# Kernel tuning notes

Hardware: AMD Instinct MI355X
Metric: run time of the kernel (lower is better)

Reference implementation:

```python
import jax, jax.numpy as jnp
import numpy as np

N_HEADS = 16

def setup_inputs() -> dict:
    key = jax.random.key(0)
    ks = jax.random.split(key, 9)
    B, L, D = 4, 2048, 1024
    s = D ** -0.5
    return {
        "x": jax.random.normal(ks[0], (B, L, D), dtype=jnp.float32),
        "Wq": jax.random.normal(ks[1], (D, D), dtype=jnp.float32) * s,
        "bq": jax.random.normal(ks[2], (D,), dtype=jnp.float32) * 0.02,
        "Wk": jax.random.normal(ks[3], (D, D), dtype=jnp.float32) * s,
        "bk": jax.random.normal(ks[4], (D,), dtype=jnp.float32) * 0.02,
        "Wv": jax.random.normal(ks[5], (D, D), dtype=jnp.float32) * s,
        "bv": jax.random.normal(ks[6], (D,), dtype=jnp.float32) * 0.02,
        "Wo": jax.random.normal(ks[7], (D, D), dtype=jnp.float32) * s,
        "bo": jax.random.normal(ks[8], (D,), dtype=jnp.float32) * 0.02,
    }

def reference(x, Wq, bq, Wk, bk, Wv, bv, Wo, bo):
    B, L, D = x.shape
    H = N_HEADS
    hd = D // H
    scale = hd ** -0.5
    # torch Linear: y = x @ W.T + b
    q = (x @ Wq.T + bq).reshape(B, L, H, hd)
    k = (x @ Wk.T + bk).reshape(B, L, H, hd)
    v = (x @ Wv.T + bv).reshape(B, L, H, hd)
    # scores [B,H,L,L]
    qk = jnp.einsum('bqhd,bkhd->bhqk', q, k) * scale
    causal = jnp.tril(jnp.ones((L, L), dtype=bool))
    qk = jnp.where(causal[None, None, :, :], qk, -jnp.inf)
    attn = jax.nn.softmax(qk, axis=-1)
    out = jnp.einsum('bhqk,bkhd->bqhd', attn, v).reshape(B, L, D)
    return out @ Wo.T + bo
```

## Files before the change

kernel.cpp:

```cpp
#include <hip/hip_runtime.h>
#include <hip/hip_bf16.h>
#include <math.h>

#define Bsz 4
#define Lsz 2048
#define Dsz 1024
#define Hn 16
#define HDsz 64
#define NQT 16

typedef __attribute__((ext_vector_type(8))) short short8;
typedef __attribute__((ext_vector_type(4))) float floatx4;
typedef unsigned short ushort_t;

__device__ __forceinline__ void load_lds_16B(const void* g, void* l) {
    __builtin_amdgcn_global_load_lds(
        (const __attribute__((address_space(1))) unsigned int*)g,
        (__attribute__((address_space(3))) unsigned int*)l, 16, 0, 0);
}

__device__ inline void cvt_store(float* p, size_t i, float v) { p[i] = v; }
__device__ inline void cvt_store(__hip_bfloat16* p, size_t i, float v) {
    p[i] = __float2bfloat16(v);
}

__device__ inline ushort_t f2bf_raw(float f) {
    __hip_bfloat16 b = __float2bfloat16(f);
    return *reinterpret_cast<ushort_t*>(&b);
}

__device__ inline float bf2f_raw(ushort_t u) {
    union { unsigned int i; float f; } c;
    c.i = ((unsigned int)u) << 16;
    return c.f;
}

__device__ __forceinline__ float fast_exp2(float x) {
#if __has_builtin(__builtin_amdgcn_exp2f)
    return __builtin_amdgcn_exp2f(x);
#else
    return exp2f(x);
#endif
}

__device__ __forceinline__ unsigned pk_bf16_rhu(float p0, float p1) {
    return __builtin_amdgcn_perm(__builtin_bit_cast(unsigned, p1) + 0x8000u,
                                 __builtin_bit_cast(unsigned, p0) + 0x8000u,
                                 0x07060302u);
}

__global__ __launch_bounds__(256) void f2ball(
    const float* __restrict__ x, const float* __restrict__ w0,
    const float* __restrict__ w1, const float* __restrict__ w2,
    const float* __restrict__ w3, __hip_bfloat16* __restrict__ xb,
    __hip_bfloat16* __restrict__ wb) {
    int bid = blockIdx.x;
    const float* in;
    __hip_bfloat16* o;
    size_t off;
    if (bid < 8192) {
        off = (size_t)bid * 1024 + threadIdx.x * 4;
        in = x;
        o = xb + off;
    } else {
        int b2 = bid - 8192;
        int sel = b2 >> 10;
        in = sel == 0 ? w0 : (sel == 1 ? w1 : (sel == 2 ? w2 : w3));
        off = (size_t)(b2 & 1023) * 1024 + threadIdx.x * 4;
        o = wb + (size_t)sel * (1024 * 1024) + off;
    }
    float4 v = *(const float4*)(in + off);
    o[0] = __float2bfloat16(v.x);
    o[1] = __float2bfloat16(v.y);
    o[2] = __float2bfloat16(v.z);
    o[3] = __float2bfloat16(v.w);
}

template <typename TO, bool QKV>
__global__ __launch_bounds__(512, 2) void gemm_bt_256(
    const ushort_t* __restrict__ A, const ushort_t* __restrict__ W,
    const float* __restrict__ b0, const float* __restrict__ b1,
    const float* __restrict__ b2, TO* __restrict__ C, int M, int N, int K) {
    __shared__ ushort_t As[2][256 * 64];
    __shared__ ushort_t Bs[2][128 * 64];

    const int t = threadIdx.x;
    const int wave = t >> 6, lane = t & 63;
    const int lmod = lane & 15, quad = lane >> 4;
    const int wm = wave >> 2, wn = wave & 3;

    const int nbn = N >> 7;
    const int nwg = nbn * (M >> 8);
    const int bid = blockIdx.x;
    const int wg = (bid & 7) * (nwg >> 3) + (bid >> 3);
    const int n0 = (wg % nbn) * 128, m0 = (wg / nbn) * 256;

    floatx4 acc[2][2][4] = {};
    short8 Af[4][2], Bf[2];

    const int NT = K >> 6;

    auto stageA = [&](int kt, int bi) {
        const int kk = kt << 6;
#pragma unroll
        for (int p = 0; p < 4; p++) {
            int slot = t + p * 512;
            int row = slot >> 3, c8 = slot & 7;
            int gc8 = c8 ^ (row & 7);
            load_lds_16B(A + (size_t)(m0 + row) * K + kk + gc8 * 8,
                         &As[bi][slot * 8]);
        }
    };
    auto stageB = [&](int kt, int bi) {
        const int kk = kt << 6;
#pragma unroll
        for (int p = 0; p < 2; p++) {
            int slot = t + p * 512;
            int row = slot >> 3, c8 = slot & 7;
            int gc8 = c8 ^ (row & 7);
            load_lds_16B(W + (size_t)(n0 + row) * K + kk + gc8 * 8,
                         &Bs[bi][slot * 8]);
        }
    };
    auto rdA = [&](int bi, int mh) {
#pragma unroll
        for (int mr = 0; mr < 4; mr++) {
            int row = wm * 128 + mh * 64 + mr * 16 + lmod;
#pragma unroll
            for (int ks = 0; ks < 2; ks++) {
                int sc8 = (ks * 4 + quad) ^ (row & 7);
                Af[mr][ks] = *(const short8*)&As[bi][row * 64 + sc8 * 8];
            }
        }
    };
    auto rdB = [&](int bi, int nh) {
        int row = wn * 32 + nh * 16 + lmod;
#pragma unroll
        for (int ks = 0; ks < 2; ks++) {
            int sc8 = (ks * 4 + quad) ^ (row & 7);
            Bf[ks] = *(const short8*)&Bs[bi][row * 64 + sc8 * 8];
        }
    };
    auto domm = [&](int mh, int nh) {
        __builtin_amdgcn_s_setprio(1);
#pragma unroll
        for (int mr = 0; mr < 4; mr++)
#pragma unroll
            for (int ks = 0; ks < 2; ks++)
                acc[mh][nh][mr] = __builtin_amdgcn_mfma_f32_16x16x32_bf16(
                    Af[mr][ks], Bf[ks], acc[mh][nh][mr], 0, 0, 0);
        __builtin_amdgcn_s_setprio(0);
    };

    stageA(0, 0);
    stageB(0, 0);
    asm volatile("s_waitcnt vmcnt(0)" ::: "memory");
    __builtin_amdgcn_s_barrier();
    asm volatile("" ::: "memory");

#pragma unroll 1
    for (int T = 0; T < NT; T++) {
        const int cur = T & 1, nxt = cur ^ 1;
        const bool pf = (T + 1 < NT);
        rdA(cur, 0);
        rdB(cur, 0);
        if (pf) stageA(T + 1, nxt);
        __builtin_amdgcn_s_barrier();
        __builtin_amdgcn_sched_barrier(0);
        domm(0, 0);
        __builtin_amdgcn_s_barrier();
        rdB(cur, 1);
        if (pf) stageB(T + 1, nxt);
        __builtin_amdgcn_s_barrier();
        __builtin_amdgcn_sched_barrier(0);
        domm(0, 1);
        __builtin_amdgcn_s_barrier();
        rdA(cur, 1);
        __builtin_amdgcn_s_barrier();
        __builtin_amdgcn_sched_barrier(0);
        domm(1, 1);
        __builtin_amdgcn_s_barrier();
        rdB(cur, 0);
        __builtin_amdgcn_s_barrier();
        __builtin_amdgcn_sched_barrier(0);
        domm(1, 0);
        asm volatile("s_waitcnt vmcnt(0)" ::: "memory");
        __builtin_amdgcn_s_barrier();
        asm volatile("" ::: "memory");
    }

    const int sec = QKV ? (n0 >> 10) : 0;
    const float* bp = QKV ? (sec == 0 ? b0 : (sec == 1 ? b1 : b2)) : b0;
    TO* Cb = QKV ? (C + (size_t)sec * M * 1024) : C;
    const int Nout = QKV ? 1024 : N;
    const float sc = (QKV && sec == 0) ? 0.1803368801111204f : 1.0f;

#pragma unroll
    for (int mh = 0; mh < 2; mh++)
#pragma unroll
        for (int mr = 0; mr < 4; mr++) {
            int gm = m0 + wm * 128 + mh * 64 + mr * 16 + quad * 4;
#pragma unroll
            for (int nh = 0; nh < 2; nh++) {
                int gn = n0 + wn * 32 + nh * 16 + lmod;
                int cn = QKV ? (gn & 1023) : gn;
                float b = bp[cn];
#pragma unroll
                for (int r = 0; r < 4; r++)
                    cvt_store(Cb, (size_t)(gm + r) * Nout + cn,
                              (acc[mh][nh][mr][r] + b) * sc);
            }
        }
}

__global__ __launch_bounds__(256) void attn_mfma(
    const ushort_t* __restrict__ q, const ushort_t* __restrict__ k,
    const ushort_t* __restrict__ v, ushort_t* __restrict__ Opart,
    float* __restrict__ lpart) {
    __shared__ ushort_t Ks[2][64 * 64];
    __shared__ ushort_t Vts[64 * 64];
    __shared__ ushort_t Ps[4][32 * 64];

    const int t = threadIdx.x;
    const int wave = t >> 6, lane = t & 63;
    const int lmod = lane & 15, quad = lane >> 4;

    const int bid = blockIdx.x;
    const int j = bid >> 3;
    const int bx = j & 15;
    const int p = bx & 7, s = bx >> 3;
    const int bh = (bid & 7) + ((j >> 4) << 3);
    const int b = bh >> 4, h = bh & 15;
    const size_t base = ((size_t)b * Lsz) * Dsz + h * HDsz;

    const int vrp = t & 31, vcg = t >> 5;
    ushort_t* Pw = (ushort_t*)Ps[wave];
    const int lm7 = lmod & 7;

    auto stageK = [&](int kt, int bi) {
#pragma unroll
        for (int pp = 0; pp < 2; pp++) {
            int slot = t + pp * 256;
            int row = slot >> 3, c8 = slot & 7;
            int gc8 = c8 ^ (row & 7);
            load_lds_16B(k + base + (size_t)(kt * 64 + row) * Dsz + gc8 * 8,
                         &Ks[bi][slot * 8]);
        }
    };
    auto loadV = [&](int kt, uint4& r0, uint4& r1) {
        const ushort_t* v0p =
            v + base + (size_t)(kt * 64 + 2 * vrp) * Dsz + vcg * 8;
        r0 = *(const uint4*)v0p;
        r1 = *(const uint4*)(v0p + Dsz);
    };
    auto writeV = [&](uint4 r0, uint4 r1) {
        unsigned vv0[4] = {r0.x, r0.y, r0.z, r0.w};
        unsigned vv1[4] = {r1.x, r1.y, r1.z, r1.w};
        const int kk = 2 * vrp;
        const int kc8 = kk >> 3, klo = kk & 7;
#pragma unroll
        for (int jj = 0; jj < 4; jj++) {
            int d0 = vcg * 8 + 2 * jj;
            unsigned lo = __builtin_amdgcn_perm(vv1[jj], vv0[jj], 0x05040100u);
            unsigned hi = __builtin_amdgcn_perm(vv1[jj], vv0[jj], 0x07060302u);
            *(unsigned*)&Vts[d0 * 64 + (kc8 ^ (d0 & 7)) * 8 + klo] = lo;
            int d1 = d0 + 1;
            *(unsigned*)&Vts[d1 * 64 + (kc8 ^ (d1 & 7)) * 8 + klo] = hi;
        }
    };

    int bi = 0;
    uint4 vr0, vr1;

    {
        const int kt00 = s * (NQT - p);
        stageK(kt00, 0);
        loadV(kt00, vr0, vr1);
    }

#pragma unroll 1
    for (int seg = 0; seg < 2; seg++) {
        const int qtile = seg == 0 ? (NQT - 1 - p) : p;
        const int q0 = qtile * 128;
        const int Th = qtile + 1;
        const int kt0 = s * Th, kt1 = kt0 + Th;
        const int kt0n = s * (p + 1);

        short8 aq[2][2];
#pragma unroll
        for (int g = 0; g < 2; g++) {
            const ushort_t* qp = q + base +
                                 (size_t)(q0 + wave * 32 + g * 16 + lmod) * Dsz +
                                 quad * 8;
            aq[g][0] = *(const short8*)(qp);
            aq[g][1] = *(const short8*)(qp + 32);
        }

        floatx4 Oacc[2][4] = {};
        float lsum[2] = {0.f, 0.f};

#pragma unroll 1
        for (int kt = kt0; kt < kt1; kt++) {
            asm volatile("s_waitcnt vmcnt(0)" ::: "memory");
            __builtin_amdgcn_s_barrier();
            asm volatile("" ::: "memory");

            writeV(vr0, vr1);
            asm volatile("s_waitcnt lgkmcnt(0)" ::: "memory");
            __builtin_amdgcn_s_barrier();
            asm volatile("" ::: "memory");

            const int ktn = (kt + 1 < kt1) ? kt + 1 : (seg == 0 ? kt0n : -1);
            if (ktn >= 0) stageK(ktn, bi ^ 1);

            floatx4 St[2][4] = {};
#pragma unroll
            for (int nt = 0; nt < 4; nt++) {
                int key = nt * 16 + lmod;
#pragma unroll
                for (int ks = 0; ks < 2; ks++) {
                    int sc8 = (ks * 4 + quad) ^ (key & 7);
                    short8 kf = *(const short8*)&Ks[bi][(key * 8 + sc8) * 8];
#pragma unroll
                    for (int g = 0; g < 2; g++)
                        St[g][nt] = __builtin_amdgcn_mfma_f32_16x16x32_bf16(
                            kf, aq[g][ks], St[g][nt], 0, 0, 0);
                }
            }

            const bool need_mask = (kt >= 2 * qtile);
#pragma unroll
            for (int g = 0; g < 2; g++) {
                int qg = q0 + wave * 32 + g * 16 + lmod;
#pragma unroll
                for (int nt = 0; nt < 4; nt++) {
                    int k0g = kt * 64 + nt * 16 + quad * 4;
                    float p0 = fast_exp2(St[g][nt][0]);
                    float p1 = fast_exp2(St[g][nt][1]);
                    float p2 = fast_exp2(St[g][nt][2]);
                    float p3 = fast_exp2(St[g][nt][3]);
                    if (need_mask) {
                        if (k0g + 0 > qg) p0 = 0.f;
                        if (k0g + 1 > qg) p1 = 0.f;
                        if (k0g + 2 > qg) p2 = 0.f;
                        if (k0g + 3 > qg) p3 = 0.f;
                    }
                    lsum[g] += ((p0 + p1) + (p2 + p3));
                    uint2 w;
                    w.x = pk_bf16_rhu(p0, p1);
                    w.y = pk_bf16_rhu(p2, p3);
                    int c8 = nt * 2 + (quad >> 1);
                    int sc8 = c8 ^ lm7;
                    *(uint2*)&Pw[((g * 16 + lmod) * 8 + sc8) * 8 +
                                 (quad & 1) * 4] = w;
                }
            }

            if (ktn >= 0) loadV(ktn, vr0, vr1);

            short8 ap[2][2];
#pragma unroll
            for (int g = 0; g < 2; g++)
#pragma unroll
                for (int ks = 0; ks < 2; ks++) {
                    int sc8 = (ks * 4 + quad) ^ lm7;
                    ap[g][ks] =
                        *(const short8*)&Pw[((g * 16 + lmod) * 8 + sc8) * 8];
                }
#pragma unroll
            for (int on = 0; on < 4; on++) {
                int d = on * 16 + lmod;
#pragma unroll
                for (int ks = 0; ks < 2; ks++) {
                    int sc8 = (ks * 4 + quad) ^ (d & 7);
                    short8 bv = *(const short8*)&Vts[(d * 8 + sc8) * 8];
#pragma unroll
                    for (int g = 0; g < 2; g++)
                        Oacc[g][on] = __builtin_amdgcn_mfma_f32_16x16x32_bf16(
                            ap[g][ks], bv, Oacc[g][on], 0, 0, 0);
                }
            }

            bi ^= 1;
        }

#pragma unroll
        for (int g = 0; g < 2; g++) {
            lsum[g] += __shfl_xor(lsum[g], 16);
            lsum[g] += __shfl_xor(lsum[g], 32);
        }

        const size_t rec = ((size_t)bh * NQT + qtile) * 2 + s;
        ushort_t* Orec = Opart + rec * (128 * 64);
        float* lrec = lpart + rec * 128;
#pragma unroll
        for (int g = 0; g < 2; g++) {
            if (quad == 0) lrec[wave * 32 + g * 16 + lmod] = lsum[g];
#pragma unroll
            for (int r = 0; r < 4; r++) {
                int row = wave * 32 + g * 16 + quad * 4 + r;
#pragma unroll
                for (int on = 0; on < 4; on++) {
                    int d = on * 16 + lmod;
                    Orec[row * 64 + d] = f2bf_raw(Oacc[g][on][r]);
                }
            }
        }
    }
}

__global__ __launch_bounds__(256) void attn_combine(
    const ushort_t* __restrict__ Opart, const float* __restrict__ lpart,
    ushort_t* __restrict__ ao) {
    int gidx = blockIdx.x * 256 + threadIdx.x;
    int rowglob = gidx >> 3;
    int c8 = (gidx & 7) * 8;
    int bh = rowglob >> 11;
    int r11 = rowglob & 2047;
    int qtile = r11 >> 7, row = r11 & 127;

    size_t rec0 = ((size_t)bh * NQT + qtile) * 2;
    const ushort_t* O0 = Opart + (rec0 + 0) * (128 * 64) + row * 64 + c8;
    const ushort_t* O1 = Opart + (rec0 + 1) * (128 * 64) + row * 64 + c8;
    float l = lpart[(rec0 + 0) * 128 + row] + lpart[(rec0 + 1) * 128 + row];
    float inv = 1.0f / l;

    short8 a = *(const short8*)O0;
    short8 bvec = *(const short8*)O1;
    short8 o;
#pragma unroll
    for (int j = 0; j < 8; j++) {
        float vv = (bf2f_raw((ushort_t)a[j]) + bf2f_raw((ushort_t)bvec[j])) * inv;
        o[j] = (short)f2bf_raw(vv);
    }
    int b = bh >> 4, h = bh & 15;
    int qg = qtile * 128 + row;
    *(short8*)&ao[((size_t)(b * Lsz + qg)) * Dsz + h * HDsz + c8] = o;
}

extern "C" void kernel_launch(void* const* d_in, const int* in_sizes, int n_in,
                              void* d_out, int out_size, void* d_ws,
                              size_t ws_size, hipStream_t stream) {
    const size_t elems = (size_t)Bsz * Lsz * Dsz;
    const size_t welem = (size_t)Dsz * Dsz;
    const size_t nrec = (size_t)Bsz * Hn * NQT * 2;
    const size_t opart_e = nrec * 128 * 64;
    const size_t need = (5 * elems + 4 * welem + opart_e) * 2 + nrec * 128 * 4;
    if (ws_size < need) return;

    const float* x = (const float*)d_in[0];
    const float* Wq = (const float*)d_in[1];
    const float* bq = (const float*)d_in[2];
    const float* Wk = (const float*)d_in[3];
    const float* bk = (const float*)d_in[4];
    const float* Wv = (const float*)d_in[5];
    const float* bv = (const float*)d_in[6];
    const float* Wo = (const float*)d_in[7];
    const float* bo = (const float*)d_in[8];
    float* out = (float*)d_out;

    __hip_bfloat16* xb = (__hip_bfloat16*)d_ws;
    __hip_bfloat16* q = xb + elems;
    __hip_bfloat16* k = q + elems;
    __hip_bfloat16* v = k + elems;
    __hip_bfloat16* ao = v + elems;
    __hip_bfloat16* Wqb = ao + elems;
    __hip_bfloat16* Wkb = Wqb + welem;
    __hip_bfloat16* Wvb = Wkb + welem;
    __hip_bfloat16* Wob = Wvb + welem;
    ushort_t* Opart = (ushort_t*)(Wob + welem);
    float* lpart = (float*)(Opart + opart_e);

    const int M = Bsz * Lsz, N = Dsz, K = Dsz;

    f2ball<<<12288, 256, 0, stream>>>(x, Wq, Wk, Wv, Wo, xb, Wqb);

    gemm_bt_256<__hip_bfloat16, true><<<(3 * N / 128) * (M / 256), 512, 0,
                                        stream>>>(
        (const ushort_t*)xb, (const ushort_t*)Wqb, bq, bk, bv, q, M, 3 * N, K);

    attn_mfma<<<16 * Bsz * Hn, 256, 0, stream>>>(
        (const ushort_t*)q, (const ushort_t*)k, (const ushort_t*)v, Opart,
        lpart);

    attn_combine<<<(int)(elems / 8 / 256), 256, 0, stream>>>(Opart, lpart,
                                                             (ushort_t*)ao);

    gemm_bt_256<float, false><<<(N / 128) * (M / 256), 512, 0, stream>>>(
        (const ushort_t*)ao, (const ushort_t*)Wob, bo, bo, bo, out, M, N, K);
}
```

Before: 279.5 us.

## Stage V via async LDS loads and read transposed with ds_read_b64_tr_b16

V tiles were loaded into registers, transposed with perm instructions and written to LDS, which needed an extra barrier per key tile. They are now copied straight from global memory into a swizzled LDS buffer with global_load_lds, and the PV MFMA operands are read with the transposing ds_read_b64_tr_b16 instruction from precomputed addresses. Probability packing also switches from manual round-half-up to the hardware v_cvt_pk_bf16_f32 instruction. This removes VGPR staging and one barrier, but the V load is now issued in the same iteration it is consumed, with a vmcnt wait before PV, so less latency is hidden.

```diff
diff --git a/kernel.cpp b/kernel.cpp
--- a/kernel.cpp
+++ b/kernel.cpp
@@ -11,6 +11,7 @@
 
 typedef __attribute__((ext_vector_type(8))) short short8;
 typedef __attribute__((ext_vector_type(4))) float floatx4;
+typedef __attribute__((ext_vector_type(2))) unsigned uint2v;
 typedef unsigned short ushort_t;
 
 __device__ __forceinline__ void load_lds_16B(const void* g, void* l) {
@@ -41,12 +42,6 @@
 #else
     return exp2f(x);
 #endif
-}
-
-__device__ __forceinline__ unsigned pk_bf16_rhu(float p0, float p1) {
-    return __builtin_amdgcn_perm(__builtin_bit_cast(unsigned, p1) + 0x8000u,
-                                 __builtin_bit_cast(unsigned, p0) + 0x8000u,
-                                 0x07060302u);
 }
 
 __global__ __launch_bounds__(256) void f2ball(
@@ -218,7 +213,7 @@
     const ushort_t* __restrict__ v, ushort_t* __restrict__ Opart,
     float* __restrict__ lpart) {
     __shared__ ushort_t Ks[2][64 * 64];
-    __shared__ ushort_t Vts[64 * 64];
+    __shared__ ushort_t Vs[64 * 64];
     __shared__ ushort_t Ps[4][32 * 64];
 
     const int t = threadIdx.x;
@@ -233,7 +228,6 @@
     const int b = bh >> 4, h = bh & 15;
     const size_t base = ((size_t)b * Lsz) * Dsz + h * HDsz;
 
-    const int vrp = t & 31, vcg = t >> 5;
     ushort_t* Pw = (ushort_t*)Ps[wave];
     const int lm7 = lmod & 7;
 
@@ -247,36 +241,40 @@
                          &Ks[bi][slot * 8]);
         }
     };
-    auto loadV = [&](int kt, uint4& r0, uint4& r1) {
-        const ushort_t* v0p =
-            v + base + (size_t)(kt * 64 + 2 * vrp) * Dsz + vcg * 8;
-        r0 = *(const uint4*)v0p;
-        r1 = *(const uint4*)(v0p + Dsz);
-    };
-    auto writeV = [&](uint4 r0, uint4 r1) {
-        unsigned vv0[4] = {r0.x, r0.y, r0.z, r0.w};
-        unsigned vv1[4] = {r1.x, r1.y, r1.z, r1.w};
-        const int kk = 2 * vrp;
-        const int kc8 = kk >> 3, klo = kk & 7;
-#pragma unroll
-        for (int jj = 0; jj < 4; jj++) {
-            int d0 = vcg * 8 + 2 * jj;
-            unsigned lo = __builtin_amdgcn_perm(vv1[jj], vv0[jj], 0x05040100u);
-            unsigned hi = __builtin_amdgcn_perm(vv1[jj], vv0[jj], 0x07060302u);
-            *(unsigned*)&Vts[d0 * 64 + (kc8 ^ (d0 & 7)) * 8 + klo] = lo;
-            int d1 = d0 + 1;
-            *(unsigned*)&Vts[d1 * 64 + (kc8 ^ (d1 & 7)) * 8 + klo] = hi;
-        }
-    };
+    auto stageV = [&](int kt) {
+#pragma unroll
+        for (int pp = 0; pp < 2; pp++) {
+            int slot = t + pp * 256;
+            int row = slot >> 3, c8 = slot & 7;
+            int gc8 = c8 ^ (row & 7);
+            load_lds_16B(v + base + (size_t)(kt * 64 + row) * Dsz + gc8 * 8,
+                         &Vs[slot * 8]);
+        }
+    };
+
+    const unsigned vsbase =
+        (unsigned)(size_t)(__attribute__((address_space(3))) const ushort_t*)Vs;
+    unsigned vaddr[2][2][4];
+    {
+        const int lq = lmod >> 2;
+        const int lmb = (lmod & 3) >> 1;
+        const int lob = (lmod & 1) * 8;
+#pragma unroll
+        for (int ks = 0; ks < 2; ks++)
+#pragma unroll
+            for (int jj = 0; jj < 2; jj++) {
+                int rowk = ks * 32 + quad * 8 + jj * 4 + lq;
+                int r7 = rowk & 7;
+#pragma unroll
+                for (int on = 0; on < 4; on++)
+                    vaddr[ks][jj][on] = vsbase + rowk * 128 +
+                                        (((on * 2 + lmb) ^ r7) << 4) + lob;
+            }
+    }
 
     int bi = 0;
-    uint4 vr0, vr1;
-
-    {
-        const int kt00 = s * (NQT - p);
-        stageK(kt00, 0);
-        loadV(kt00, vr0, vr1);
-    }
+
+    stageK(s * (NQT - p), 0);
 
 #pragma unroll 1
     for (int seg = 0; seg < 2; seg++) {
@@ -305,11 +303,7 @@
             __builtin_amdgcn_s_barrier();
             asm volatile("" ::: "memory");
 
-            writeV(vr0, vr1);
-            asm volatile("s_waitcnt lgkmcnt(0)" ::: "memory");
-            __builtin_amdgcn_s_barrier();
-            asm volatile("" ::: "memory");
-
+            stageV(kt);
             const int ktn = (kt + 1 < kt1) ? kt + 1 : (seg == 0 ? kt0n : -1);
             if (ktn >= 0) stageK(ktn, bi ^ 1);
 
@@ -346,9 +340,16 @@
                         if (k0g + 3 > qg) p3 = 0.f;
                     }
                     lsum[g] += ((p0 + p1) + (p2 + p3));
+                    unsigned wx, wy;
+                    asm("v_cvt_pk_bf16_f32 %0, %1, %2"
+                        : "=v"(wx)
+                        : "v"(p0), "v"(p1));
+                    asm("v_cvt_pk_bf16_f32 %0, %1, %2"
+                        : "=v"(wy)
+                        : "v"(p2), "v"(p3));
                     uint2 w;
-                    w.x = pk_bf16_rhu(p0, p1);
-                    w.y = pk_bf16_rhu(p2, p3);
+                    w.x = wx;
+                    w.y = wy;
                     int c8 = nt * 2 + (quad >> 1);
                     int sc8 = c8 ^ lm7;
                     *(uint2*)&Pw[((g * 16 + lmod) * 8 + sc8) * 8 +
@@ -356,8 +357,6 @@
                 }
             }
 
-            if (ktn >= 0) loadV(ktn, vr0, vr1);
-
             short8 ap[2][2];
 #pragma unroll
             for (int g = 0; g < 2; g++)
@@ -367,17 +366,42 @@
                     ap[g][ks] =
                         *(const short8*)&Pw[((g * 16 + lmod) * 8 + sc8) * 8];
                 }
+
+            if (ktn >= 0)
+                asm volatile("s_waitcnt vmcnt(2)" ::: "memory");
+            else
+                asm volatile("s_waitcnt vmcnt(0)" ::: "memory");
+            __builtin_amdgcn_s_barrier();
+            asm volatile("" ::: "memory");
+
 #pragma unroll
             for (int on = 0; on < 4; on++) {
-                int d = on * 16 + lmod;
-#pragma unroll
-                for (int ks = 0; ks < 2; ks++) {
-                    int sc8 = (ks * 4 + quad) ^ (d & 7);
-                    short8 bv = *(const short8*)&Vts[(d * 8 + sc8) * 8];
-#pragma unroll
-                    for (int g = 0; g < 2; g++)
-                        Oacc[g][on] = __builtin_amdgcn_mfma_f32_16x16x32_bf16(
-                            ap[g][ks], bv, Oacc[g][on], 0, 0, 0);
+                uint2v t00, t01, t10, t11;
+                asm volatile("ds_read_b64_tr_b16 %0, %1"
+                             : "=v"(t00)
+                             : "v"(vaddr[0][0][on]));
+                asm volatile("ds_read_b64_tr_b16 %0, %1"
+                             : "=v"(t01)
+                             : "v"(vaddr[0][1][on]));
+                asm volatile("ds_read_b64_tr_b16 %0, %1"
+                             : "=v"(t10)
+                             : "v"(vaddr[1][0][on]));
+                asm volatile("ds_read_b64_tr_b16 %0, %1"
+                             : "=v"(t11)
+                             : "v"(vaddr[1][1][on]));
+                asm volatile("s_waitcnt lgkmcnt(0)" ::: "memory");
+                __builtin_amdgcn_sched_barrier(0);
+                union U { uint2v pr[2]; short8 s8; } u0, u1;
+                u0.pr[0] = t00;
+                u0.pr[1] = t01;
+                u1.pr[0] = t10;
+                u1.pr[1] = t11;
+#pragma unroll
+                for (int g = 0; g < 2; g++) {
+                    Oacc[g][on] = __builtin_amdgcn_mfma_f32_16x16x32_bf16(
+                        ap[g][0], u0.s8, Oacc[g][on], 0, 0, 0);
+                    Oacc[g][on] = __builtin_amdgcn_mfma_f32_16x16x32_bf16(
+                        ap[g][1], u1.s8, Oacc[g][on], 0, 0, 0);
                 }
             }
 
```

Measured after the change: 279.3 us. Within noise of the previous version (-0.1%).
